# Performance work log

Measured on AMD Instinct MI355X. Metric: run time of the kernel, lower is better.

The kernel has to match this reference:

```python
import jax, jax.numpy as jnp
import numpy as np
import math

DIM = 768
HEADS = 12
HEAD_DIM = DIM // HEADS
SCALE_PARAM_INIT = 1.0 / math.sqrt(DIM)  # Scale(scale=1/sqrt(dim), init=1.0)


def cosine_norm(x, eps=1e-6):
    norm = jnp.maximum(jnp.linalg.norm(x, axis=-1, keepdims=True), eps)
    return x / norm


def setup_inputs() -> dict:
    key = jax.random.key(0)
    ks = jax.random.split(key, 6)
    B, N = 8, 1024
    x = jax.random.normal(ks[0], (B, N, DIM), dtype=jnp.float32)
    # torch nn.Linear weights are [out, in]; y = x @ W^T
    std = 1.0 / math.sqrt(DIM)
    Wq = jax.random.uniform(ks[1], (DIM, DIM), jnp.float32, -std, std)
    Wk = jax.random.uniform(ks[2], (DIM, DIM), jnp.float32, -std, std)
    Wv = jax.random.uniform(ks[3], (DIM, DIM), jnp.float32, -std, std)
    Wo = jax.random.uniform(ks[4], (DIM, DIM), jnp.float32, -std, std)
    # Scale param s: ones * scale, perturbed slightly for generality
    s_qk = SCALE_PARAM_INIT * (1.0 + 0.1 * jax.random.normal(ks[5], (HEADS, HEAD_DIM), jnp.float32))
    return {"x": x, "Wq": Wq, "Wk": Wk, "Wv": Wv, "Wo": Wo, "s_qk": s_qk}


def reference(x, Wq, Wk, Wv, Wo, s_qk):
    B, N, _ = x.shape
    # projections (torch Linear: x @ W^T)
    q = (x @ Wq.T).reshape(B, N, HEADS, HEAD_DIM)
    k = (x @ Wk.T).reshape(B, N, HEADS, HEAD_DIM)
    v = (x @ Wv.T).reshape(B, N, HEADS, HEAD_DIM)
    # effective scale = s * (init / scale)
    s_eff = s_qk * (1.0 / SCALE_PARAM_INIT)  # [H, D]
    q = cosine_norm(q) * s_eff  # broadcast over [B, N, H, D]
    k = cosine_norm(k) * s_eff
    scale = HEAD_DIM ** 0.5  # note: multiplies logits (nGPT-style)
    # [B, H, N, N]
    logits = jnp.einsum('bqhd,bkhd->bhqk', q, k) * scale
    attn = jax.nn.softmax(logits, axis=-1)
    out = jnp.einsum('bhqk,bkhd->bqhd', attn, v).reshape(B, N, HEADS * HEAD_DIM)
    return out @ Wo.T
```

## Files before the change

kernel.cpp:

```cpp
#include <hip/hip_runtime.h>
#include <hip/hip_bf16.h>
#include <math.h>

#define NDIM 768
#define NHEADS 12
#define HD 64
#define SEQ 1024
#define BATCH 8
#define MROWS (BATCH * SEQ)
#define SQRT_DIM 27.712812921102035f
#define LOG2E 1.4426950408889634f

typedef unsigned short u16;
typedef unsigned int u32;
typedef __attribute__((ext_vector_type(8))) short short8;
typedef __attribute__((ext_vector_type(4))) short bf16x4;
typedef __attribute__((ext_vector_type(4))) float f32x4;
typedef __attribute__((ext_vector_type(16))) float f32x16;
typedef __attribute__((ext_vector_type(2))) u32 u32x2;
typedef __attribute__((ext_vector_type(4))) u32 u32x4;

#define MFMA16(a, b, c) __builtin_amdgcn_mfma_f32_16x16x32_bf16(a, b, c, 0, 0, 0)
#define MFMA32(a, b, c) __builtin_amdgcn_mfma_f32_32x32x16_bf16(a, b, c, 0, 0, 0)

#if __has_builtin(__builtin_amdgcn_exp2f)
#define EXP2(x) __builtin_amdgcn_exp2f(x)
#else
#define EXP2(x) exp2f(x)
#endif

__device__ inline u16 f2bf(float f) {
    __hip_bfloat16 h = __float2bfloat16(f);
    return *reinterpret_cast<u16*>(&h);
}

__device__ inline u32 rne_pack(float a, float b) {
    u32 ua = __builtin_bit_cast(u32, a), ub = __builtin_bit_cast(u32, b);
    ua = (ua + 0x7fffu + ((ua >> 16) & 1u)) >> 16;
    ub = (ub + 0x7fffu + ((ub >> 16) & 1u)) >> 16;
    return (ub << 16) | ua;
}

__device__ inline u32 cvtpk(float a, float b) {
    u32 r;
    asm("v_cvt_pk_bf16_f32 %0, %1, %2" : "=v"(r) : "v"(a), "v"(b));
    return r;
}

__device__ inline void gl2lds16(const void* g, void* l) {
    __builtin_amdgcn_global_load_lds((const __attribute__((address_space(1))) void*)g,
                                     (__attribute__((address_space(3))) void*)l, 16, 0, 0);
}

__device__ inline void bar() {
    asm volatile("" ::: "memory");
    __builtin_amdgcn_s_barrier();
    asm volatile("" ::: "memory");
}
#define LGKM0 asm volatile("s_waitcnt lgkmcnt(0)" ::: "memory")
#define VM0   asm volatile("s_waitcnt vmcnt(0)" ::: "memory")

__device__ inline void plswap(u32 a, u32 b, int half, u32& x, u32& y) {
#if __has_builtin(__builtin_amdgcn_permlane32_swap)
    u32x2 r = __builtin_amdgcn_permlane32_swap(a, b, false, false);
    x = r[0]; y = r[1];
#else
    u32 oa = __shfl_xor(a, 32, 64), ob = __shfl_xor(b, 32, 64);
    x = half ? ob : a;
    y = half ? b : oa;
#endif
}

__global__ __launch_bounds__(256) void castall(const float* __restrict__ x,
                                               const float* __restrict__ Wq,
                                               const float* __restrict__ Wk,
                                               const float* __restrict__ Wv,
                                               const float* __restrict__ Wo,
                                               u16* __restrict__ xb,
                                               u16* __restrict__ Wqkv,
                                               u16* __restrict__ Wob) {
    const int WB = (NDIM * NDIM) / 1024;
    int blk = blockIdx.x;
    const float* s;
    u16* d;
    int base;
    if (blk < 6144) {
        s = x; d = xb; base = blk * 1024;
    } else {
        int wsel = (blk - 6144) / WB, r = (blk - 6144) % WB;
        base = r * 1024;
        if (wsel == 0)      { s = Wq; d = Wqkv; }
        else if (wsel == 1) { s = Wk; d = Wqkv + NDIM * NDIM; }
        else if (wsel == 2) { s = Wv; d = Wqkv + 2 * NDIM * NDIM; }
        else                { s = Wo; d = Wob; }
    }
    int i = base + threadIdx.x * 4;
    float4 v = *(const float4*)(s + i);
    uint2 o = make_uint2(rne_pack(v.x, v.y), rne_pack(v.z, v.w));
    *(uint2*)(d + i) = o;
}

__global__ __launch_bounds__(512, 2) void gemm256_qkv(const u16* __restrict__ A,
                                                      const u16* __restrict__ B,
                                                      u16* __restrict__ Vt,
                                                      const float* __restrict__ s_qk,
                                                      u16* __restrict__ Qdst,
                                                      u16* __restrict__ Kdst) {
    constexpr int K = NDIM;
    constexpr int NT = K / 64;
    __shared__ __align__(16) u16 As[2][2][128 * 64];
    __shared__ __align__(16) u16 Bs[2][2][128 * 64];

    const int t = threadIdx.x;
    const int wave = t >> 6, lane = t & 63;
    const int quad = lane >> 4, l16 = lane & 15;
    const int fx = l16 & 7;
    const int blk = blockIdx.x;

    const int srow = lane >> 3;
    const int schk = (lane & 7) ^ srow;
    auto stg = [&](const u16* src, u16* dst) {
#pragma unroll
        for (int it = 0; it < 2; ++it) {
            const int cb = it * 512 + wave * 64;
            const int r = (cb >> 3) + srow;
            gl2lds16(src + (size_t)r * K + schk * 8, (char*)dst + cb * 16);
        }
    };

    const int wm = wave >> 2, wn = wave & 3;
    const int xcd = blk & 7, local = blk >> 3;
    const int bm = xcd * 1024 + (local >> 3) * 256;
    const int bn = (local & 7) * 256;

    f32x4 acc[8][4];
#pragma unroll
    for (int i = 0; i < 8; ++i)
#pragma unroll
        for (int j = 0; j < 4; ++j) acc[i][j] = (f32x4){0.f, 0.f, 0.f, 0.f};

    const u16* Ag = A + (size_t)bm * K;
    const u16* Bg = B + (size_t)bn * K;

    stg(Ag,                        As[0][0]);
    stg(Ag + (size_t)128 * K,      As[0][1]);
    stg(Bg,                        Bs[0][0]);
    stg(Bg + (size_t)128 * K,      Bs[0][1]);
    stg(Bg + 64,                   Bs[1][0]);
    stg(Bg + (size_t)128 * K + 64, Bs[1][1]);
    asm volatile("s_waitcnt vmcnt(4)" ::: "memory");
    bar();

    short8 a[4][2], b0[2][2], b1[2][2];
    const int rb0 = (wn & 1) * 64;

#pragma unroll 2
    for (int T = 0; T < NT; ++T) {
        const int db = T & 1;
        u16* Asl = As[db][wm];
        u16* Bsl = Bs[db][wn >> 1];
        const u16* An = Ag + (size_t)(T + 1) * 64;
        const u16* Bn = Bg + (size_t)(T + 2) * 64;

#pragma unroll
        for (int mi = 0; mi < 4; ++mi) {
            const int r = mi * 16 + l16;
#pragma unroll
            for (int kk = 0; kk < 2; ++kk)
                a[mi][kk] = *(const short8*)&Asl[(r * 8 + ((kk * 4 + quad) ^ fx)) * 8];
        }
#pragma unroll
        for (int ni = 0; ni < 2; ++ni) {
            const int r = rb0 + ni * 16 + l16;
#pragma unroll
            for (int kk = 0; kk < 2; ++kk)
                b0[ni][kk] = *(const short8*)&Bsl[(r * 8 + ((kk * 4 + quad) ^ fx)) * 8];
        }
        if (T + 1 < NT) stg(An, As[db ^ 1][0]);
        bar();
        LGKM0;
        __builtin_amdgcn_s_setprio(1);
#pragma unroll
        for (int kk = 0; kk < 2; ++kk)
#pragma unroll
            for (int mi = 0; mi < 4; ++mi)
#pragma unroll
                for (int ni = 0; ni < 2; ++ni)
                    acc[mi][ni] = MFMA16(a[mi][kk], b0[ni][kk], acc[mi][ni]);
        __builtin_amdgcn_s_setprio(0);
        bar();

#pragma unroll
        for (int ni = 0; ni < 2; ++ni) {
            const int r = rb0 + (ni + 2) * 16 + l16;
#pragma unroll
            for (int kk = 0; kk < 2; ++kk)
                b1[ni][kk] = *(const short8*)&Bsl[(r * 8 + ((kk * 4 + quad) ^ fx)) * 8];
        }
        if (T + 1 < NT) stg(An + (size_t)128 * K, As[db ^ 1][1]);
        bar();
        LGKM0;
        __builtin_amdgcn_s_setprio(1);
#pragma unroll
        for (int kk = 0; kk < 2; ++kk)
#pragma unroll
            for (int mi = 0; mi < 4; ++mi)
#pragma unroll
                for (int ni = 0; ni < 2; ++ni)
                    acc[mi][ni + 2] = MFMA16(a[mi][kk], b1[ni][kk], acc[mi][ni + 2]);
        __builtin_amdgcn_s_setprio(0);
        bar();

#pragma unroll
        for (int mi = 0; mi < 4; ++mi) {
            const int r = (mi + 4) * 16 + l16;
#pragma unroll
            for (int kk = 0; kk < 2; ++kk)
                a[mi][kk] = *(const short8*)&Asl[(r * 8 + ((kk * 4 + quad) ^ fx)) * 8];
        }
        if (T + 2 < NT) stg(Bn, Bs[db][0]);
        bar();
        LGKM0;
        __builtin_amdgcn_s_setprio(1);
#pragma unroll
        for (int kk = 0; kk < 2; ++kk)
#pragma unroll
            for (int mi = 0; mi < 4; ++mi)
#pragma unroll
                for (int ni = 0; ni < 2; ++ni)
                    acc[mi + 4][ni + 2] = MFMA16(a[mi][kk], b1[ni][kk], acc[mi + 4][ni + 2]);
        __builtin_amdgcn_s_setprio(0);
        bar();

        if (T + 2 < NT) stg(Bn + (size_t)128 * K, Bs[db][1]);
        bar();
        __builtin_amdgcn_s_setprio(1);
#pragma unroll
        for (int kk = 0; kk < 2; ++kk)
#pragma unroll
            for (int mi = 0; mi < 4; ++mi)
#pragma unroll
                for (int ni = 0; ni < 2; ++ni)
                    acc[mi + 4][ni] = MFMA16(a[mi][kk], b0[ni][kk], acc[mi + 4][ni]);
        __builtin_amdgcn_s_setprio(0);
        if (T + 2 < NT) {
            asm volatile("s_waitcnt vmcnt(4)" ::: "memory");
        } else {
            VM0;
        }
        bar();
    }

    const int cg = (bn + wn * 64) >> 6;
    if (cg >= 2 * NHEADS) {
        const int h = cg - 2 * NHEADS;
#pragma unroll
        for (int mi = 0; mi < 8; ++mi) {
            const int row = bm + wm * 128 + mi * 16 + quad * 4;
            const int bb = row >> 10, n0 = row & 1023;
#pragma unroll
            for (int ni = 0; ni < 4; ++ni) {
                const int dd = ni * 16 + l16;
                uint2 pk = make_uint2(rne_pack(acc[mi][ni][0], acc[mi][ni][1]),
                                      rne_pack(acc[mi][ni][2], acc[mi][ni][3]));
                *(uint2*)(Vt + (((size_t)(bb * NHEADS + h) * HD + dd) << 10) + n0) = pk;
            }
        }
    } else {
        const bool isq = cg < NHEADS;
        const int h = isq ? cg : cg - NHEADS;
        u16* dst = isq ? Qdst : Kdst;
        const float ex = isq ? 8.f * LOG2E : 1.f;
        float sq[4];
#pragma unroll
        for (int ni = 0; ni < 4; ++ni)
            sq[ni] = s_qk[h * HD + ni * 16 + l16] * SQRT_DIM * ex;
#pragma unroll
        for (int mi = 0; mi < 8; ++mi)
#pragma unroll
            for (int r = 0; r < 4; ++r) {
                float ss = 0.f;
#pragma unroll
                for (int ni = 0; ni < 4; ++ni) ss += acc[mi][ni][r] * acc[mi][ni][r];
                ss += __shfl_xor(ss, 1, 64);
                ss += __shfl_xor(ss, 2, 64);
                ss += __shfl_xor(ss, 4, 64);
                ss += __shfl_xor(ss, 8, 64);
                float inv = 1.f / fmaxf(sqrtf(ss), 1e-6f);
                const int row = bm + wm * 128 + mi * 16 + quad * 4 + r;
                const int bb = row >> 10, tok = row & 1023;
                u16* o = dst + ((size_t)(bb * NHEADS + h) * SEQ + tok) * HD;
#pragma unroll
                for (int ni = 0; ni < 4; ++ni)
                    o[ni * 16 + l16] = f2bf(acc[mi][ni][r] * sq[ni] * inv);
            }
    }
}

__global__ __launch_bounds__(512, 4) void vtail(const u16* __restrict__ A,
                                                const u16* __restrict__ B,
                                                u16* __restrict__ Vt) {
    constexpr int K = NDIM;
    constexpr int NT = K / 64;
    __shared__ __align__(16) u16 Ar[3][64 * 64];
    __shared__ __align__(16) u16 Br[3][128 * 64];

    const int t = threadIdx.x;
    const int wave = t >> 6, lane = t & 63;
    const int quad = lane >> 4, l16 = lane & 15;
    const int fx = l16 & 7;
    const int srow = lane >> 3;
    const int schk = (lane & 7) ^ srow;

    const int q = blockIdx.x;
    const int bm = (q >> 1) * 64;
    const int bcol = (q & 1) * 128;
    const int wm2 = wave >> 2;
    const int wn4 = wave & 3;
    const u16* Ag = A + (size_t)bm * K;
    const u16* Bg = B + (size_t)(2048 + bcol) * K;

    auto stage = [&](int Tk, int s) {
        {
            const int cb = wave * 64;
            const int r = (cb >> 3) + srow;
            gl2lds16(Ag + (size_t)r * K + Tk * 64 + schk * 8,
                     (char*)Ar[s] + cb * 16);
        }
#pragma unroll
        for (int it = 0; it < 2; ++it) {
            const int cb = it * 512 + wave * 64;
            const int r = (cb >> 3) + srow;
            gl2lds16(Bg + (size_t)r * K + Tk * 64 + schk * 8,
                     (char*)Br[s] + cb * 16);
        }
    };

    f32x4 acc[2][2];
#pragma unroll
    for (int i = 0; i < 2; ++i)
#pragma unroll
        for (int j = 0; j < 2; ++j) acc[i][j] = (f32x4){0.f, 0.f, 0.f, 0.f};

    stage(0, 0);
    stage(1, 1);
#pragma unroll
    for (int T = 0; T < NT; ++T) {
        if (T + 1 < NT) asm volatile("s_waitcnt vmcnt(3)" ::: "memory");
        else            VM0;
        bar();
        if (T + 2 < NT) stage(T + 2, (T + 2) % 3);
        const u16* Asl = Ar[T % 3];
        const u16* Bsl = Br[T % 3];
        short8 af[2][2], bf[2][2];
#pragma unroll
        for (int mi = 0; mi < 2; ++mi) {
            const int r = wm2 * 32 + mi * 16 + l16;
#pragma unroll
            for (int kk = 0; kk < 2; ++kk)
                af[mi][kk] = *(const short8*)&Asl[(r * 8 + ((kk * 4 + quad) ^ fx)) * 8];
        }
#pragma unroll
        for (int ni = 0; ni < 2; ++ni) {
            const int r = wn4 * 32 + ni * 16 + l16;
#pragma unroll
            for (int kk = 0; kk < 2; ++kk)
                bf[ni][kk] = *(const short8*)&Bsl[(r * 8 + ((kk * 4 + quad) ^ fx)) * 8];
        }
        __builtin_amdgcn_s_setprio(1);
#pragma unroll
        for (int kk = 0; kk < 2; ++kk)
#pragma unroll
            for (int mi = 0; mi < 2; ++mi)
#pragma unroll
                for (int ni = 0; ni < 2; ++ni)
                    acc[mi][ni] = MFMA16(af[mi][kk], bf[ni][kk], acc[mi][ni]);
        __builtin_amdgcn_s_setprio(0);
    }

#pragma unroll
    for (int mi = 0; mi < 2; ++mi) {
        const int row0 = bm + wm2 * 32 + mi * 16 + quad * 4;
        const int bb = row0 >> 10, n0 = row0 & 1023;
#pragma unroll
        for (int ni = 0; ni < 2; ++ni) {
            const int cv = bcol + wn4 * 32 + ni * 16 + l16;
            const int h = 8 + (cv >> 6), dd = cv & 63;
            uint2 pk = make_uint2(rne_pack(acc[mi][ni][0], acc[mi][ni][1]),
                                  rne_pack(acc[mi][ni][2], acc[mi][ni][3]));
            *(uint2*)(Vt + (((size_t)(bb * NHEADS + h) * HD + dd) << 10) + n0) = pk;
        }
    }
}

template <int EPI>
__global__ __launch_bounds__(256) void gemm_bf16(const u16* __restrict__ A,
                                                 const u16* __restrict__ B,
                                                 void* __restrict__ C, int N,
                                                 const float* __restrict__ s_qk,
                                                 u16* __restrict__ Qdst,
                                                 u16* __restrict__ Kdst,
                                                 int NX) {
    constexpr int K = NDIM;
    constexpr int NKT = K / 32;
    __shared__ __align__(16) u16 As[2][4096];
    __shared__ __align__(16) u16 Bs[2][4096];
    const int t = threadIdx.x;
    const int wave = t >> 6, lane = t & 63;
    const int quad = lane >> 4, l16 = lane & 15;
    const int wx = (wave & 1) * 64, wy = (wave >> 1) * 64;
    const int blk = blockIdx.x;
    const int xcd = blk & 7, local = blk >> 3;
    const int bm = (xcd * 8 + local / NX) * 128;
    const int bn = (local % NX) * 128;

    f32x4 acc[4][4];
#pragma unroll
    for (int i = 0; i < 4; ++i)
#pragma unroll
        for (int j = 0; j < 4; ++j) acc[i][j] = (f32x4){0.f, 0.f, 0.f, 0.f};

    const int srl = lane >> 2;
    const int skc = (lane & 3) ^ ((lane >> 3) & 3);
    auto stage = [&](int k0, int bsel) {
#pragma unroll
        for (int it = 0; it < 2; ++it) {
            const int cb = it * 256 + wave * 64;
            const int row = (cb >> 6) * 16 + srl;
            gl2lds16(A + (size_t)(bm + row) * K + k0 + skc * 8,
                     (char*)As[bsel] + cb * 16);
            gl2lds16(B + (size_t)(bn + row) * K + k0 + skc * 8,
                     (char*)Bs[bsel] + cb * 16);
        }
    };
    const int fxor = (l16 >> 1) & 3;

    stage(0, 0);
#pragma unroll
    for (int kt = 0; kt < NKT; ++kt) {
        __syncthreads();
        if (kt + 1 < NKT) stage((kt + 1) * 32, (kt + 1) & 1);
        const int b = kt & 1;
        short8 af[4], bfr[4];
#pragma unroll
        for (int i = 0; i < 4; ++i)
            af[i] = *(const short8*)&As[b][
                ((((wy >> 4) + i) * 64 + l16 * 4 + (quad ^ fxor)) * 8)];
#pragma unroll
        for (int j = 0; j < 4; ++j)
            bfr[j] = *(const short8*)&Bs[b][
                ((((wx >> 4) + j) * 64 + l16 * 4 + (quad ^ fxor)) * 8)];
#pragma unroll
        for (int i = 0; i < 4; ++i)
#pragma unroll
            for (int j = 0; j < 4; ++j) acc[i][j] = MFMA16(af[i], bfr[j], acc[i][j]);
    }

    if constexpr (EPI == 0) {
#pragma unroll
        for (int i = 0; i < 4; ++i)
#pragma unroll
            for (int j = 0; j < 4; ++j)
#pragma unroll
                for (int r = 0; r < 4; ++r) {
                    const int row = bm + wy + i * 16 + quad * 4 + r;
                    const int col = bn + wx + j * 16 + l16;
                    ((float*)C)[(size_t)row * N + col] = acc[i][j][r];
                }
    }
}

__global__ __launch_bounds__(256, 3) void attn_mfma(const u16* __restrict__ Qh,
                                                    const u16* __restrict__ Kh,
                                                    const u16* __restrict__ Vt,
                                                    u16* __restrict__ AO) {
    __shared__ __align__(16) u16 Ks[2][512 * 8];
    __shared__ __align__(16) u16 Vs[2][512 * 8];

    const int t = threadIdx.x;
    const int wave = t >> 6, lane = t & 63;
    const int l31 = lane & 31, half = lane >> 5;

    const int bid = blockIdx.x;
    const int xcd = bid & 7, idx = bid >> 3;
    const int bh = xcd * 12 + (idx % 12);
    const int q0 = (idx / 12) * 128;
    const int b = bh / NHEADS, h = bh - b * NHEADS;

    const u16* Kb = Kh + (size_t)bh * SEQ * HD;
    const u16* Vb = Vt + (size_t)bh * HD * SEQ;
    const int qb = q0 + wave * 32;

    short8 qf[4];
#pragma unroll
    for (int tt = 0; tt < 4; ++tt)
        qf[tt] = *(const short8*)(Qh + ((size_t)bh * SEQ + qb + l31) * HD +
                                  tt * 16 + half * 8);

    f32x16 o[2];
#pragma unroll
    for (int dt = 0; dt < 2; ++dt)
#pragma unroll
        for (int r = 0; r < 16; ++r) o[dt][r] = 0.f;
    float lp = 0.f;

    const int arl = lane >> 3;
    const int acc8 = (lane & 7) ^ arl;
    const int fx8 = l31 & 7;

    auto stage = [&](int j0, int db) {
#pragma unroll
        for (int it = 0; it < 2; ++it) {
            const int cb = it * 256 + wave * 64;
            const int r0 = (cb >> 6) * 8 + arl;
            gl2lds16(Kb + (size_t)(j0 + r0) * HD + acc8 * 8,
                     (char*)Ks[db] + cb * 16);
            gl2lds16(Vb + (size_t)r0 * SEQ + j0 + acc8 * 8,
                     (char*)Vs[db] + cb * 16);
        }
    };

    stage(0, 0);
#pragma unroll 2
    for (int jt = 0; jt < SEQ / 64; ++jt) {
        const int db = jt & 1;
        VM0;
        bar();
        if (jt + 1 < SEQ / 64) stage((jt + 1) * 64, db ^ 1);
        const u16* Ksl = Ks[db];
        const u16* Vsl = Vs[db];

        f32x16 sa0, sa1;
#pragma unroll
        for (int r = 0; r < 16; ++r) { sa0[r] = 0.f; sa1[r] = 0.f; }
#pragma unroll
        for (int tt = 0; tt < 4; ++tt) {
            short8 kf0 = *(const short8*)&Ksl[
                ((((l31 >> 3)) * 64) + fx8 * 8 + ((2 * tt + half) ^ fx8)) * 8];
            short8 kf1 = *(const short8*)&Ksl[
                (((4 + (l31 >> 3)) * 64) + fx8 * 8 + ((2 * tt + half) ^ fx8)) * 8];
            sa0 = MFMA32(kf0, qf[tt], sa0);
            sa1 = MFMA32(kf1, qf[tt], sa1);
        }

        short8 pf0a, pf0b, pf1a, pf1b;
        {
            float p[16];
#pragma unroll
            for (int r = 0; r < 16; ++r) p[r] = EXP2(sa0[r]);
#pragma unroll
            for (int rg = 0; rg < 4; ++rg)
                lp += (p[rg * 4] + p[rg * 4 + 1]) + (p[rg * 4 + 2] + p[rg * 4 + 3]);
            u32 q[8];
#pragma unroll
            for (int i = 0; i < 8; ++i) q[i] = cvtpk(p[2 * i], p[2 * i + 1]);
            u32 d0, d1, d2, d3, e0, e1, e2, e3;
            plswap(q[0], q[2], half, d0, d2);
            plswap(q[1], q[3], half, d1, d3);
            plswap(q[4], q[6], half, e0, e2);
            plswap(q[5], q[7], half, e1, e3);
            u32x4 f0v = {d0, d1, d2, d3};
            u32x4 f1v = {e0, e1, e2, e3};
            pf0a = __builtin_bit_cast(short8, f0v);
            pf0b = __builtin_bit_cast(short8, f1v);
        }
        {
            float p[16];
#pragma unroll
            for (int r = 0; r < 16; ++r) p[r] = EXP2(sa1[r]);
#pragma unroll
            for (int rg = 0; rg < 4; ++rg)
                lp += (p[rg * 4] + p[rg * 4 + 1]) + (p[rg * 4 + 2] + p[rg * 4 + 3]);
            u32 q[8];
#pragma unroll
            for (int i = 0; i < 8; ++i) q[i] = cvtpk(p[2 * i], p[2 * i + 1]);
            u32 d0, d1, d2, d3, e0, e1, e2, e3;
            plswap(q[0], q[2], half, d0, d2);
            plswap(q[1], q[3], half, d1, d3);
            plswap(q[4], q[6], half, e0, e2);
            plswap(q[5], q[7], half, e1, e3);
            u32x4 f0v = {d0, d1, d2, d3};
            u32x4 f1v = {e0, e1, e2, e3};
            pf1a = __builtin_bit_cast(short8, f0v);
            pf1b = __builtin_bit_cast(short8, f1v);
        }

#pragma unroll
        for (int kt = 0; kt < 2; ++kt)
#pragma unroll
            for (int s = 0; s < 2; ++s) {
                short8 pf = kt ? (s ? pf1b : pf1a) : (s ? pf0b : pf0a);
                const int c = kt * 4 + s * 2 + half;
#pragma unroll
                for (int dt = 0; dt < 2; ++dt) {
                    short8 vf = *(const short8*)&Vsl[
                        (((dt * 4 + (l31 >> 3)) * 64) + fx8 * 8 + (c ^ fx8)) * 8];
                    o[dt] = MFMA32(vf, pf, o[dt]);
                }
            }
    }

    const float invl = 1.f / (lp + __shfl_xor(lp, 32, 64));
    u16* ob = AO + (size_t)(b * SEQ + qb + l31) * NDIM + h * HD;
#pragma unroll
    for (int dt = 0; dt < 2; ++dt)
#pragma unroll
        for (int rg = 0; rg < 4; ++rg) {
            bf16x4 ok = {(short)f2bf(o[dt][rg * 4 + 0] * invl),
                         (short)f2bf(o[dt][rg * 4 + 1] * invl),
                         (short)f2bf(o[dt][rg * 4 + 2] * invl),
                         (short)f2bf(o[dt][rg * 4 + 3] * invl)};
            *(bf16x4*)(ob + dt * 32 + rg * 8 + half * 4) = ok;
        }
}

extern "C" void kernel_launch(void* const* d_in, const int* in_sizes, int n_in,
                              void* d_out, int out_size, void* d_ws, size_t ws_size,
                              hipStream_t stream) {
    const float* x    = (const float*)d_in[0];
    const float* Wq   = (const float*)d_in[1];
    const float* Wk   = (const float*)d_in[2];
    const float* Wv   = (const float*)d_in[3];
    const float* Wo   = (const float*)d_in[4];
    const float* s_qk = (const float*)d_in[5];
    float* out = (float*)d_out;

    char* w = (char*)d_ws;
    const size_t TE = (size_t)MROWS * NDIM;
    u16* xb   = (u16*)w;                    w += TE * 2;
    u16* Wqkv = (u16*)w;                    w += (size_t)3 * NDIM * NDIM * 2;
    u16* Wob  = (u16*)w;                    w += (size_t)NDIM * NDIM * 2;
    u16* Qh   = (u16*)w;                    w += TE * 2;
    u16* Kh   = (u16*)w;                    w += TE * 2;
    u16* Vt   = (u16*)w;                    w += TE * 2;
    u16* ao   = (u16*)w;

    castall<<<6144 + 4 * 576, 256, 0, stream>>>(x, Wq, Wk, Wv, Wo, xb, Wqkv, Wob);

    gemm256_qkv<<<256, 512, 0, stream>>>(xb, Wqkv, Vt, s_qk, Qh, Kh);

    vtail<<<256, 512, 0, stream>>>(xb, Wqkv, Vt);

    attn_mfma<<<768, 256, 0, stream>>>(Qh, Kh, Vt, ao);

    gemm_bf16<0><<<6 * 64, 256, 0, stream>>>(
        ao, Wob, out, NDIM, nullptr, nullptr, nullptr, 6);
}
```

Measured before the change: 175.1 us.

## Rewrite output projection GEMM with 64x128 tiles and triple-buffered K=64 pipeline

Replaces the generic 128x128 double-buffered output-projection GEMM with a dedicated kernel that uses 64x128 tiles, 512 threads, and K-steps of 64. Loads are triple-buffered with explicit vmcnt waits, and MFMA issue is wrapped in setprio. The grid doubles from 384 to 768 blocks to better fill the CUs, and the XOR swizzle is reworked for 64-wide rows. The cost is lower per-block data reuse, since the smaller M tile means more total global traffic for the weights.

After: 175.9 us. Within noise of the previous version (+0.5%).

```diff
diff --git a/kernel.cpp b/kernel.cpp
--- a/kernel.cpp
+++ b/kernel.cpp
@@ -393,80 +393,98 @@
     }
 }
 
-template <int EPI>
-__global__ __launch_bounds__(256) void gemm_bf16(const u16* __restrict__ A,
-                                                 const u16* __restrict__ B,
-                                                 void* __restrict__ C, int N,
-                                                 const float* __restrict__ s_qk,
-                                                 u16* __restrict__ Qdst,
-                                                 u16* __restrict__ Kdst,
-                                                 int NX) {
+__global__ __launch_bounds__(512, 4) void oproj(const u16* __restrict__ A,
+                                                const u16* __restrict__ B,
+                                                float* __restrict__ C) {
     constexpr int K = NDIM;
-    constexpr int NKT = K / 32;
-    __shared__ __align__(16) u16 As[2][4096];
-    __shared__ __align__(16) u16 Bs[2][4096];
+    constexpr int NT = K / 64;
+    __shared__ __align__(16) u16 Ar[3][64 * 64];
+    __shared__ __align__(16) u16 Br[3][128 * 64];
+
     const int t = threadIdx.x;
     const int wave = t >> 6, lane = t & 63;
     const int quad = lane >> 4, l16 = lane & 15;
-    const int wx = (wave & 1) * 64, wy = (wave >> 1) * 64;
-    const int blk = blockIdx.x;
-    const int xcd = blk & 7, local = blk >> 3;
-    const int bm = (xcd * 8 + local / NX) * 128;
-    const int bn = (local % NX) * 128;
-
-    f32x4 acc[4][4];
-#pragma unroll
-    for (int i = 0; i < 4; ++i)
-#pragma unroll
-        for (int j = 0; j < 4; ++j) acc[i][j] = (f32x4){0.f, 0.f, 0.f, 0.f};
-
-    const int srl = lane >> 2;
-    const int skc = (lane & 3) ^ ((lane >> 3) & 3);
-    auto stage = [&](int k0, int bsel) {
+    const int fx = l16 & 7;
+    const int srow = lane >> 3;
+    const int schk = (lane & 7) ^ srow;
+
+    const int bid = blockIdx.x;
+    const int xcd = bid & 7, idx = bid >> 3;
+    const int bm = (xcd * 16 + idx / 6) * 64;
+    const int bn = (idx % 6) * 128;
+    const int wm2 = wave >> 2;
+    const int wn4 = wave & 3;
+    const u16* Ag = A + (size_t)bm * K;
+    const u16* Bg = B + (size_t)bn * K;
+
+    auto stage = [&](int Tk, int s) {
+        {
+            const int cb = wave * 64;
+            const int r = (cb >> 3) + srow;
+            gl2lds16(Ag + (size_t)r * K + Tk * 64 + schk * 8,
+                     (char*)Ar[s] + cb * 16);
+        }
 #pragma unroll
         for (int it = 0; it < 2; ++it) {
-            const int cb = it * 256 + wave * 64;
-            const int row = (cb >> 6) * 16 + srl;
-            gl2lds16(A + (size_t)(bm + row) * K + k0 + skc * 8,
-                     (char*)As[bsel] + cb * 16);
-            gl2lds16(B + (size_t)(bn + row) * K + k0 + skc * 8,
-                     (char*)Bs[bsel] + cb * 16);
+            const int cb = it * 512 + wave * 64;
+            const int r = (cb >> 3) + srow;
+            gl2lds16(Bg + (size_t)r * K + Tk * 64 + schk * 8,
+                     (char*)Br[s] + cb * 16);
         }
     };
-    const int fxor = (l16 >> 1) & 3;
+
+    f32x4 acc[2][2];
+#pragma unroll
+    for (int i = 0; i < 2; ++i)
+#pragma unroll
+        for (int j = 0; j < 2; ++j) acc[i][j] = (f32x4){0.f, 0.f, 0.f, 0.f};
 
     stage(0, 0);
-#pragma unroll
-    for (int kt = 0; kt < NKT; ++kt) {
-        __syncthreads();
-        if (kt + 1 < NKT) stage((kt + 1) * 32, (kt + 1) & 1);
-        const int b = kt & 1;
-        short8 af[4], bfr[4];
-#pragma unroll
-        for (int i = 0; i < 4; ++i)
-            af[i] = *(const short8*)&As[b][
-                ((((wy >> 4) + i) * 64 + l16 * 4 + (quad ^ fxor)) * 8)];
-#pragma unroll
-        for (int j = 0; j < 4; ++j)
-            bfr[j] = *(const short8*)&Bs[b][
-                ((((wx >> 4) + j) * 64 + l16 * 4 + (quad ^ fxor)) * 8)];
-#pragma unroll
-        for (int i = 0; i < 4; ++i)
-#pragma unroll
-            for (int j = 0; j < 4; ++j) acc[i][j] = MFMA16(af[i], bfr[j], acc[i][j]);
-    }
-
-    if constexpr (EPI == 0) {
-#pragma unroll
-        for (int i = 0; i < 4; ++i)
-#pragma unroll
-            for (int j = 0; j < 4; ++j)
-#pragma unroll
-                for (int r = 0; r < 4; ++r) {
-                    const int row = bm + wy + i * 16 + quad * 4 + r;
-                    const int col = bn + wx + j * 16 + l16;
-                    ((float*)C)[(size_t)row * N + col] = acc[i][j][r];
-                }
+    stage(1, 1);
+#pragma unroll
+    for (int T = 0; T < NT; ++T) {
+        if (T + 1 < NT) asm volatile("s_waitcnt vmcnt(3)" ::: "memory");
+        else            VM0;
+        bar();
+        if (T + 2 < NT) stage(T + 2, (T + 2) % 3);
+        const u16* Asl = Ar[T % 3];
+        const u16* Bsl = Br[T % 3];
+        short8 af[2][2], bf[2][2];
+#pragma unroll
+        for (int mi = 0; mi < 2; ++mi) {
+            const int r = wm2 * 32 + mi * 16 + l16;
+#pragma unroll
+            for (int kk = 0; kk < 2; ++kk)
+                af[mi][kk] = *(const short8*)&Asl[(r * 8 + ((kk * 4 + quad) ^ fx)) * 8];
+        }
+#pragma unroll
+        for (int ni = 0; ni < 2; ++ni) {
+            const int r = wn4 * 32 + ni * 16 + l16;
+#pragma unroll
+            for (int kk = 0; kk < 2; ++kk)
+                bf[ni][kk] = *(const short8*)&Bsl[(r * 8 + ((kk * 4 + quad) ^ fx)) * 8];
+        }
+        __builtin_amdgcn_s_setprio(1);
+#pragma unroll
+        for (int kk = 0; kk < 2; ++kk)
+#pragma unroll
+            for (int mi = 0; mi < 2; ++mi)
+#pragma unroll
+                for (int ni = 0; ni < 2; ++ni)
+                    acc[mi][ni] = MFMA16(af[mi][kk], bf[ni][kk], acc[mi][ni]);
+        __builtin_amdgcn_s_setprio(0);
+    }
+
+#pragma unroll
+    for (int mi = 0; mi < 2; ++mi) {
+        const int row0 = bm + wm2 * 32 + mi * 16 + quad * 4;
+#pragma unroll
+        for (int ni = 0; ni < 2; ++ni) {
+            const int col = bn + wn4 * 32 + ni * 16 + l16;
+#pragma unroll
+            for (int r = 0; r < 4; ++r)
+                C[(size_t)(row0 + r) * NDIM + col] = acc[mi][ni][r];
+        }
     }
 }
 
@@ -643,6 +661,5 @@
 
     attn_mfma<<<768, 256, 0, stream>>>(Qh, Kh, Vt, ao);
 
-    gemm_bf16<0><<<6 * 64, 256, 0, stream>>>(
-        ao, Wob, out, NDIM, nullptr, nullptr, nullptr, 6);
-}
+    oproj<<<768, 512, 0, stream>>>(ao, Wob, out);
+}
```
